# Kernel optimization log

Hardware: AMD Instinct MI355X
Metric: run time of the kernel (lower is better)

The kernel has to match this reference:

```python
import jax, jax.numpy as jnp
import numpy as np

N = 50000          # nodes
E_RAND = 800000    # random edges (plus N self-loops)
IN, HID, OUT = 128, 32, 32
HEADS = (4, 4, 6)
NEG_SLOPE = 0.2    # DGL GATConv default leaky_relu slope


def setup_inputs() -> dict:
    key = jax.random.key(0)
    ks = jax.random.split(key, 16)
    s = 0.05
    x = jax.random.normal(ks[0], (N, IN), jnp.float32)
    # random graph + self loops (SELF_LOOP=True in the source)
    src = jnp.concatenate([jax.random.randint(ks[1], (E_RAND,), 0, N),
                           jnp.arange(N)]).astype(jnp.int32)
    dst = jnp.concatenate([jax.random.randint(ks[2], (E_RAND,), 0, N),
                           jnp.arange(N)]).astype(jnp.int32)
    H0, H1, H2 = HEADS
    return dict(
        x=x, src=src, dst=dst,
        W1=jax.random.normal(ks[3], (IN, H0 * HID), jnp.float32) * s,
        al1=jax.random.normal(ks[4], (H0, HID), jnp.float32) * s,
        ar1=jax.random.normal(ks[5], (H0, HID), jnp.float32) * s,
        b1=jnp.zeros((H0 * HID,), jnp.float32),
        W2=jax.random.normal(ks[6], (H0 * HID, H1 * HID), jnp.float32) * s,
        al2=jax.random.normal(ks[7], (H1, HID), jnp.float32) * s,
        ar2=jax.random.normal(ks[8], (H1, HID), jnp.float32) * s,
        b2=jnp.zeros((H1 * HID,), jnp.float32),
        W3=jax.random.normal(ks[9], (H1 * HID, H2 * OUT), jnp.float32) * s,
        al3=jax.random.normal(ks[10], (H2, OUT), jnp.float32) * s,
        ar3=jax.random.normal(ks[11], (H2, OUT), jnp.float32) * s,
        b3=jnp.zeros((H2 * OUT,), jnp.float32),
        resW3=jax.random.normal(ks[12], (H1 * HID, H2 * OUT), jnp.float32) * s,
    )


def gat_layer(h, src, dst, W, al, ar, b, residual=None, act_relu=True):
    """One DGL-style GATConv: fc -> per-edge leaky_relu attention -> edge
    softmax over incoming edges -> weighted scatter-sum -> (+res) + bias -> act."""
    n = h.shape[0]
    H, out = al.shape
    feat = (h @ W).reshape(n, H, out)                 # [N,H,out]
    el = jnp.sum(feat * al, axis=-1)                  # [N,H]
    er = jnp.sum(feat * ar, axis=-1)                  # [N,H]
    e = jax.nn.leaky_relu(el[src] + er[dst], NEG_SLOPE)  # [E,H]
    emax = jax.ops.segment_max(e, dst, num_segments=n)   # [N,H]
    ex = jnp.exp(e - emax[dst])                       # [E,H]
    denom = jax.ops.segment_sum(ex, dst, num_segments=n) # [N,H]
    alpha = ex / jnp.maximum(denom[dst], 1e-9)        # [E,H]
    msg = feat[src] * alpha[..., None]                # [E,H,out]
    rst = jax.ops.segment_sum(msg, dst, num_segments=n)  # [N,H,out]
    if residual is not None:
        rst = rst + residual
    rst = rst + b.reshape(1, H, out)
    return jax.nn.relu(rst) if act_relu else rst


def reference(x, src, dst, W1, al1, ar1, b1, W2, al2, ar2, b2,
              W3, al3, ar3, b3, resW3):
    n = x.shape[0]
    # layer 1: no residual, relu, flatten heads
    h1 = gat_layer(x, src, dst, W1, al1, ar1, b1).reshape(n, -1)
    # layer 2: residual is Identity (in_dim == heads*hid), relu, flatten
    res2 = h1.reshape(n, HEADS[1], HID)
    h2 = gat_layer(h1, src, dst, W2, al2, ar2, b2, residual=res2).reshape(n, -1)
    # layer 3: residual via linear projection (dims differ), no activation, mean heads
    res3 = (h2 @ resW3).reshape(n, HEADS[2], OUT)
    h3 = gat_layer(h2, src, dst, W3, al3, ar3, b3, residual=res3, act_relu=False)
    return h3.mean(axis=1)
```

## Files before the change

kernel.cpp:

```cpp
#include <hip/hip_runtime.h>
#include <math.h>


typedef _Float16 v8h __attribute__((ext_vector_type(8)));
typedef float f32x4 __attribute__((ext_vector_type(4)));

__device__ __host__ inline int pack_off(int n, int k) {
    return ((n >> 4) << 11) | ((k >> 5) << 9) | (((k >> 3) & 3) << 7) | ((n & 15) << 3) | (k & 7);
}


__global__ void hist_kernel(const int* __restrict__ dst, int E, int* __restrict__ deg) {
    int i = blockIdx.x * blockDim.x + threadIdx.x;
    if (i < E) atomicAdd(&deg[dst[i]], 1);
}

__global__ void scan_phaseA(const int* __restrict__ deg, int n, int* __restrict__ bsum) {
    __shared__ int red[4];
    int t = threadIdx.x;
    int base = blockIdx.x * 2048 + t * 8;
    int s = 0;
    #pragma unroll
    for (int q = 0; q < 8; q++) { int i = base + q; if (i < n) s += deg[i]; }
    #pragma unroll
    for (int off = 1; off < 64; off <<= 1) s += __shfl_xor(s, off);
    if ((t & 63) == 0) red[t >> 6] = s;
    __syncthreads();
    if (t == 0) bsum[blockIdx.x] = red[0] + red[1] + red[2] + red[3];
}

__global__ void scan_phaseB(int* __restrict__ bsum, int nb) {
    int lane = threadIdx.x & 63;
    int v = (lane < nb) ? bsum[lane] : 0;
    int inc = v;
    #pragma unroll
    for (int off = 1; off < 64; off <<= 1) {
        int u = __shfl_up(inc, off);
        if (lane >= off) inc += u;
    }
    int ex = inc - v;
    if (lane < nb) bsum[lane] = ex;
}

__global__ void scan_phaseC(const int* __restrict__ deg, int n, const int* __restrict__ bsum,
                            int* __restrict__ row_start, int E) {
    __shared__ int wsum[4];
    int t = threadIdx.x;
    int lane = t & 63, wv = t >> 6;
    int base = blockIdx.x * 2048 + t * 8;
    int v[8]; int s = 0;
    #pragma unroll
    for (int q = 0; q < 8; q++) { int i = base + q; v[q] = (i < n) ? deg[i] : 0; s += v[q]; }
    int inc = s;
    #pragma unroll
    for (int off = 1; off < 64; off <<= 1) {
        int u = __shfl_up(inc, off);
        if (lane >= off) inc += u;
    }
    if (lane == 63) wsum[wv] = inc;
    __syncthreads();
    int woff = 0;
    for (int w = 0; w < wv; w++) woff += wsum[w];
    int run = inc - s + woff + bsum[blockIdx.x];
    #pragma unroll
    for (int q = 0; q < 8; q++) {
        int i = base + q;
        if (i < n) row_start[i] = run;
        run += v[q];
    }
    if (blockIdx.x == 0 && t == 0) row_start[n] = E;
}

__global__ void fill_kernel(const int* __restrict__ src, const int* __restrict__ dst, int E,
                            const int* __restrict__ row_start, int* __restrict__ cursor,
                            int* __restrict__ csr_src) {
    int i = blockIdx.x * blockDim.x + threadIdx.x;
    if (i < E) {
        int d = dst[i];
        int pos = atomicAdd(&cursor[d], 1);
        csr_src[row_start[d] + pos] = src[i];
    }
}


__global__ void wsplit_all(const float* __restrict__ W1, const float* __restrict__ W2,
                           const float* __restrict__ W3, const float* __restrict__ Wr,
                           _Float16* __restrict__ o) {
    int i = blockIdx.x * blockDim.x + threadIdx.x;
    if (i >= 61440) return;
    float v; int ohi, stride, po;
    if (i < 16384) {
        int e = i, c = e >> 7, k = e & 127;
        v = W1[(size_t)k * 128 + c]; ohi = 0; stride = 16384; po = pack_off(c, k);
    } else if (i < 32768) {
        int e = i - 16384, c = e >> 7, k = e & 127;
        v = W2[(size_t)k * 128 + c]; ohi = 32768; stride = 16384; po = pack_off(c, k);
    } else if (i < 57344) {
        int e = i - 32768, c = e >> 7, k = e & 127;
        v = W3[(size_t)k * 192 + c]; ohi = 65536; stride = 28672; po = pack_off(c, k);
    } else {
        int e = i - 57344, c = e >> 7, k = e & 127;
        float s = 0.f;
        #pragma unroll
        for (int h = 0; h < 6; h++) s += Wr[(size_t)k * 192 + h * 32 + c];
        v = s * (1.0f / 6.0f);
        ohi = 65536; stride = 28672; po = 24576 + pack_off(c, k);
    }
    _Float16 hv = (_Float16)v;
    o[ohi + po] = hv;
    o[ohi + stride + po] = (_Float16)(v - (float)hv);
}


__global__ void splitx_kernel(const float* __restrict__ x, _Float16* __restrict__ hi,
                              _Float16* __restrict__ lo, int N, int PT) {
    int i = blockIdx.x * blockDim.x + threadIdx.x;
    if (i >= PT * 2048) return;
    int mt = i >> 11, r = i & 2047;
    int q4 = r >> 9, quad = (r >> 7) & 3, ln = (r >> 3) & 15, j = r & 7;
    int n = mt * 16 + ln, k = q4 * 32 + quad * 8 + j;
    float v = (n < N) ? x[(size_t)n * 128 + k] : 0.f;
    _Float16 h = (_Float16)v;
    hi[i] = h;
    lo[i] = (_Float16)(v - (float)h);
}


template <int CC, int H>
__global__ __launch_bounds__(256, 4) void mfma_fc(
    const _Float16* __restrict__ Ahi, const _Float16* __restrict__ Alo,
    const _Float16* __restrict__ Bhi, const _Float16* __restrict__ Blo,
    const float* __restrict__ al, const float* __restrict__ ar,
    _Float16* __restrict__ feat_out,
    float* __restrict__ el, float* __restrict__ er, int N) {
    constexpr int TILES = CC / 16;
    int t = threadIdx.x;
    int wave = t >> 6, lane = t & 63;
    int ln = lane & 15, quad = lane >> 4;
    int mt = blockIdx.x * 4 + wave;

    f32x4 acc[TILES];
    #pragma unroll
    for (int i = 0; i < TILES; i++) acc[i] = (f32x4){0.f, 0.f, 0.f, 0.f};

    const _Float16* pa_h = Ahi + (size_t)mt * 2048 + lane * 8;
    const _Float16* pa_l = Alo + (size_t)mt * 2048 + lane * 8;

    #pragma unroll
    for (int q4 = 0; q4 < 4; q4++) {
        v8h ah = *(const v8h*)(pa_h + q4 * 512);
        v8h av = *(const v8h*)(pa_l + q4 * 512);
        #pragma unroll
        for (int tt = 0; tt < TILES; tt++) {
            size_t boff = (size_t)tt * 2048 + q4 * 512 + lane * 8;
            v8h bh = *(const v8h*)(Bhi + boff);
            v8h bl = *(const v8h*)(Blo + boff);
            acc[tt] = __builtin_amdgcn_mfma_f32_16x16x32_f16(av, bh, acc[tt], 0, 0, 0);
            acc[tt] = __builtin_amdgcn_mfma_f32_16x16x32_f16(ah, bl, acc[tt], 0, 0, 0);
            acc[tt] = __builtin_amdgcn_mfma_f32_16x16x32_f16(ah, bh, acc[tt], 0, 0, 0);
        }
    }

    #pragma unroll
    for (int tt = 0; tt < TILES; tt++) {
        int n = tt * 16 + ln;
        int head = n >> 5, wi = n & 31;
        _Float16* fo = feat_out + (size_t)head * N * 32;
        #pragma unroll
        for (int r = 0; r < 4; r++) {
            int m = mt * 16 + quad * 4 + r;
            if (m < N) fo[(size_t)m * 32 + wi] = (_Float16)acc[tt][r];
        }
    }
    #pragma unroll
    for (int hg = 0; hg < H; hg++) {
        float a0 = al[hg * 32 + ln], a1 = al[hg * 32 + 16 + ln];
        float r0 = ar[hg * 32 + ln], r1 = ar[hg * 32 + 16 + ln];
        #pragma unroll
        for (int r = 0; r < 4; r++) {
            float pl = acc[2 * hg][r] * a0 + acc[2 * hg + 1][r] * a1;
            float pr = acc[2 * hg][r] * r0 + acc[2 * hg + 1][r] * r1;
            #pragma unroll
            for (int off = 1; off < 16; off <<= 1) {
                pl += __shfl_xor(pl, off);
                pr += __shfl_xor(pr, off);
            }
            int m = mt * 16 + quad * 4 + r;
            if (ln == 0 && m < N) {
                el[(size_t)hg * N + m] = pl;
                er[(size_t)hg * N + m] = pr;
            }
        }
    }
}


__global__ __launch_bounds__(256, 3) void mfma_fc3(
    const _Float16* __restrict__ Ahi, const _Float16* __restrict__ Alo,
    const _Float16* __restrict__ Bhi, const _Float16* __restrict__ Blo,
    const float* __restrict__ al, const float* __restrict__ ar,
    const float* __restrict__ b3,
    _Float16* __restrict__ feat_out, float* __restrict__ out,
    float* __restrict__ el, float* __restrict__ er, int N) {
    constexpr int H = 6, TILES = 14;
    int t = threadIdx.x;
    int wave = t >> 6, lane = t & 63;
    int ln = lane & 15, quad = lane >> 4;
    int mt = blockIdx.x * 4 + wave;

    f32x4 acc[TILES];
    #pragma unroll
    for (int i = 0; i < TILES; i++) acc[i] = (f32x4){0.f, 0.f, 0.f, 0.f};

    const _Float16* pa_h = Ahi + (size_t)mt * 2048 + lane * 8;
    const _Float16* pa_l = Alo + (size_t)mt * 2048 + lane * 8;

    #pragma unroll
    for (int q4 = 0; q4 < 4; q4++) {
        v8h ah = *(const v8h*)(pa_h + q4 * 512);
        v8h av = *(const v8h*)(pa_l + q4 * 512);
        #pragma unroll
        for (int tt = 0; tt < TILES; tt++) {
            size_t boff = (size_t)tt * 2048 + q4 * 512 + lane * 8;
            v8h bh = *(const v8h*)(Bhi + boff);
            v8h bl = *(const v8h*)(Blo + boff);
            acc[tt] = __builtin_amdgcn_mfma_f32_16x16x32_f16(av, bh, acc[tt], 0, 0, 0);
            acc[tt] = __builtin_amdgcn_mfma_f32_16x16x32_f16(ah, bl, acc[tt], 0, 0, 0);
            acc[tt] = __builtin_amdgcn_mfma_f32_16x16x32_f16(ah, bh, acc[tt], 0, 0, 0);
        }
    }

    #pragma unroll
    for (int tt = 0; tt < 12; tt++) {
        int n = tt * 16 + ln;
        #pragma unroll
        for (int r = 0; r < 4; r++) {
            int m = mt * 16 + quad * 4 + r;
            if (m < N) feat_out[(size_t)m * 192 + n] = (_Float16)acc[tt][r];
        }
    }
    #pragma unroll
    for (int tt = 12; tt < 14; tt++) {
        int n32 = (tt - 12) * 16 + ln;
        float bm = (b3[n32] + b3[32 + n32] + b3[64 + n32] + b3[96 + n32] +
                    b3[128 + n32] + b3[160 + n32]) * (1.0f / 6.0f);
        #pragma unroll
        for (int r = 0; r < 4; r++) {
            int m = mt * 16 + quad * 4 + r;
            if (m < N) out[(size_t)m * 32 + n32] = acc[tt][r] + bm;
        }
    }
    #pragma unroll
    for (int hg = 0; hg < H; hg++) {
        float a0 = al[hg * 32 + ln], a1 = al[hg * 32 + 16 + ln];
        float r0 = ar[hg * 32 + ln], r1 = ar[hg * 32 + 16 + ln];
        #pragma unroll
        for (int r = 0; r < 4; r++) {
            float pl = acc[2 * hg][r] * a0 + acc[2 * hg + 1][r] * a1;
            float pr = acc[2 * hg][r] * r0 + acc[2 * hg + 1][r] * r1;
            #pragma unroll
            for (int off = 1; off < 16; off <<= 1) {
                pl += __shfl_xor(pl, off);
                pr += __shfl_xor(pr, off);
            }
            int m = mt * 16 + quad * 4 + r;
            if (ln == 0 && m < N) {
                el[(size_t)hg * N + m] = pl;
                er[(size_t)hg * N + m] = pr;
            }
        }
    }
}


template <int RES>
__global__ __launch_bounds__(256) void gat_agg_q(
        const _Float16* __restrict__ feat_planes, const float* __restrict__ el,
        const float* __restrict__ er, const int* __restrict__ row_start,
        const int* __restrict__ csr_src, const float* __restrict__ bias,
        const _Float16* __restrict__ res_hi, const _Float16* __restrict__ res_lo,
        _Float16* __restrict__ out_hi, _Float16* __restrict__ out_lo,
        int N, int NB16) {
    constexpr int H = 4;
    unsigned b = blockIdx.x;
    unsigned C = (unsigned)(NB16 * H) >> 3;
    unsigned t = (b & 7u) * C + (b >> 3);
    int h  = (int)(t / (unsigned)NB16);
    int ng = (int)(t - (unsigned)h * (unsigned)NB16);
    int wv = threadIdx.x >> 6, lane = threadIdx.x & 63;
    int slice = lane >> 4, sl = lane & 15;
    int q = sl & 3;
    int g = sl >> 2;
    int n = ng * 16 + wv * 4 + slice;
    bool valid = (n < N);
    int nc = valid ? n : (N - 1);

    int start = row_start[nc];
    int end   = valid ? row_start[nc + 1] : start;
    float er_h = er[(size_t)h * N + nc];
    const float* el_h = el + (size_t)h * N;
    const _Float16* fbase = feat_planes + (size_t)h * N * 32 + q * 8;

    float acc[8];
    #pragma unroll
    for (int i = 0; i < 8; i++) acc[i] = 0.f;
    float wsum = 0.f;

    int j = start + g;
    for (; j + 4 < end; j += 8) {
        int s0 = csr_src[j];
        int s1 = csr_src[j + 4];
        float e0 = el_h[s0] + er_h;
        float e1 = el_h[s1] + er_h;
        e0 = (e0 >= 0.f) ? e0 : 0.2f * e0;
        e1 = (e1 >= 0.f) ? e1 : 0.2f * e1;
        float w0 = __expf(e0);
        float w1 = __expf(e1);
        v8h v0 = *(const v8h*)(fbase + (size_t)s0 * 32);
        v8h v1 = *(const v8h*)(fbase + (size_t)s1 * 32);
        wsum += w0 + w1;
        #pragma unroll
        for (int i = 0; i < 8; i++) acc[i] += w0 * (float)v0[i] + w1 * (float)v1[i];
    }
    if (j < end) {
        int s0 = csr_src[j];
        float e0 = el_h[s0] + er_h;
        e0 = (e0 >= 0.f) ? e0 : 0.2f * e0;
        float w0 = __expf(e0);
        v8h v0 = *(const v8h*)(fbase + (size_t)s0 * 32);
        wsum += w0;
        #pragma unroll
        for (int i = 0; i < 8; i++) acc[i] += w0 * (float)v0[i];
    }

    #pragma unroll
    for (int off = 4; off < 16; off <<= 1) {
        #pragma unroll
        for (int i = 0; i < 8; i++) acc[i] += __shfl_xor(acc[i], off);
        wsum += __shfl_xor(wsum, off);
    }

    float inv = 1.0f / fmaxf(wsum, 1e-9f);
    float4 bv0 = *(const float4*)(bias + h * 32 + q * 8);
    float4 bv1 = *(const float4*)(bias + h * 32 + q * 8 + 4);
    float r[8];
    r[0] = acc[0] * inv + bv0.x; r[1] = acc[1] * inv + bv0.y;
    r[2] = acc[2] * inv + bv0.z; r[3] = acc[3] * inv + bv0.w;
    r[4] = acc[4] * inv + bv1.x; r[5] = acc[5] * inv + bv1.y;
    r[6] = acc[6] * inv + bv1.z; r[7] = acc[7] * inv + bv1.w;

    if constexpr (RES == 1) {
        int off = pack_off(nc, h * 32 + q * 8);
        v8h rh = *(const v8h*)(res_hi + off);
        v8h rl = *(const v8h*)(res_lo + off);
        #pragma unroll
        for (int i = 0; i < 8; i++) r[i] += (float)rh[i] + (float)rl[i];
    }
    #pragma unroll
    for (int i = 0; i < 8; i++) r[i] = fmaxf(r[i], 0.f);

    if (g == 0 && valid) {
        int po = pack_off(n, h * 32 + q * 8);
        v8h hh, ll;
        #pragma unroll
        for (int i = 0; i < 8; i++) {
            hh[i] = (_Float16)r[i];
            ll[i] = (_Float16)(r[i] - (float)hh[i]);
        }
        *(v8h*)(out_hi + po) = hh;
        *(v8h*)(out_lo + po) = ll;
    }
}


__global__ __launch_bounds__(256) void gat_agg_mean6p(
        const _Float16* __restrict__ feat, const float* __restrict__ el,
        const float* __restrict__ er, const int* __restrict__ row_start,
        const int* __restrict__ csr_src, float* __restrict__ out, int N) {
    constexpr int H = 6, ROW = 192, LPG = 24, G = 2;
    int wv = threadIdx.x >> 6, lane = threadIdx.x & 63;
    int n = blockIdx.x * 4 + wv;
    if (n >= N) return;

    int d8 = lane % LPG;
    int g  = lane / LPG;
    int hd = d8 >> 2, qb = d8 & 3;

    int start = row_start[n], end = row_start[n + 1];
    float er_hd = er[(size_t)hd * N + n];
    const float* el_h = el + (size_t)hd * N;
    const _Float16* fbase = feat + 8 * d8;

    float acc[8];
    #pragma unroll
    for (int q = 0; q < 8; q++) acc[q] = 0.f;
    float wsum = 0.f;

    int j = (g < G) ? (start + g) : end;
    for (; j + 3 * G < end; j += 4 * G) {
        int s0 = csr_src[j];
        int s1 = csr_src[j + G];
        int s2 = csr_src[j + 2 * G];
        int s3 = csr_src[j + 3 * G];
        float e0 = el_h[s0] + er_hd;
        float e1 = el_h[s1] + er_hd;
        float e2 = el_h[s2] + er_hd;
        float e3 = el_h[s3] + er_hd;
        e0 = (e0 >= 0.f) ? e0 : 0.2f * e0;
        e1 = (e1 >= 0.f) ? e1 : 0.2f * e1;
        e2 = (e2 >= 0.f) ? e2 : 0.2f * e2;
        e3 = (e3 >= 0.f) ? e3 : 0.2f * e3;
        float w0 = __expf(e0);
        float w1 = __expf(e1);
        float w2 = __expf(e2);
        float w3 = __expf(e3);
        v8h v0 = *(const v8h*)(fbase + (size_t)s0 * ROW);
        v8h v1 = *(const v8h*)(fbase + (size_t)s1 * ROW);
        v8h v2 = *(const v8h*)(fbase + (size_t)s2 * ROW);
        v8h v3 = *(const v8h*)(fbase + (size_t)s3 * ROW);
        wsum += (w0 + w1) + (w2 + w3);
        #pragma unroll
        for (int q = 0; q < 8; q++)
            acc[q] += (w0 * (float)v0[q] + w1 * (float)v1[q]) +
                      (w2 * (float)v2[q] + w3 * (float)v3[q]);
    }
    for (; j < end; j += G) {
        int s0 = csr_src[j];
        float e0 = el_h[s0] + er_hd;
        e0 = (e0 >= 0.f) ? e0 : 0.2f * e0;
        float w0 = __expf(e0);
        v8h v0 = *(const v8h*)(fbase + (size_t)s0 * ROW);
        wsum += w0;
        #pragma unroll
        for (int q = 0; q < 8; q++) acc[q] += w0 * (float)v0[q];
    }

    #pragma unroll
    for (int q = 0; q < 8; q++) acc[q] += __shfl(acc[q], lane + 24);
    wsum += __shfl(wsum, lane + 24);

    float inv = 1.0f / fmaxf(wsum, 1e-9f);
    float r[8];
    #pragma unroll
    for (int q = 0; q < 8; q++) r[q] = acc[q] * inv;

    float s[8];
    #pragma unroll
    for (int q = 0; q < 8; q++) {
        s[q] = r[q];
        #pragma unroll
        for (int hh2 = 1; hh2 < H; hh2++) s[q] += __shfl(r[q], qb + 4 * hh2);
    }
    if (lane < 4) {
        const float sc = 1.0f / 6.0f;
        float4 rm0 = *(const float4*)(out + (size_t)n * 32 + 8 * lane);
        float4 rm1 = *(const float4*)(out + (size_t)n * 32 + 8 * lane + 4);
        *(float4*)(out + (size_t)n * 32 + 8 * lane) =
            make_float4(s[0] * sc + rm0.x, s[1] * sc + rm0.y,
                        s[2] * sc + rm0.z, s[3] * sc + rm0.w);
        *(float4*)(out + (size_t)n * 32 + 8 * lane + 4) =
            make_float4(s[4] * sc + rm1.x, s[5] * sc + rm1.y,
                        s[6] * sc + rm1.z, s[7] * sc + rm1.w);
    }
}


extern "C" void kernel_launch(void* const* d_in, const int* in_sizes, int n_in,
                              void* d_out, int out_size, void* d_ws, size_t ws_size,
                              hipStream_t stream) {
    const float* x    = (const float*)d_in[0];
    const int*   src  = (const int*)d_in[1];
    const int*   dst  = (const int*)d_in[2];
    const float* W1   = (const float*)d_in[3];
    const float* al1  = (const float*)d_in[4];
    const float* ar1  = (const float*)d_in[5];
    const float* b1   = (const float*)d_in[6];
    const float* W2   = (const float*)d_in[7];
    const float* al2  = (const float*)d_in[8];
    const float* ar2  = (const float*)d_in[9];
    const float* b2   = (const float*)d_in[10];
    const float* W3   = (const float*)d_in[11];
    const float* al3  = (const float*)d_in[12];
    const float* ar3  = (const float*)d_in[13];
    const float* b3   = (const float*)d_in[14];
    const float* resW3= (const float*)d_in[15];
    float* out = (float*)d_out;

    const int N = in_sizes[0] / 128;
    const int E = in_sizes[1];
    const int TILES16 = (N + 15) / 16;
    const int PT = (TILES16 + 3) & ~3;
    const int NB = PT / 4;
    const int NSB = (N + 2047) / 2048;
    const int NB16 = (TILES16 + 3) & ~3;

    float* fws  = (float*)d_ws;
    float* elb  = fws;
    float* erb  = elb + (size_t)N * 6;
    _Float16* feat_h = (_Float16*)(erb + (size_t)N * 6);
    _Float16* xh_hi  = feat_h + (size_t)N * 192;
    _Float16* xh_lo  = xh_hi + (size_t)PT * 2048;
    _Float16* h1_hi  = xh_lo + (size_t)PT * 2048;
    _Float16* h1_lo  = h1_hi + (size_t)PT * 2048;
    _Float16* wts    = h1_lo + (size_t)PT * 2048;
    int* deg       = (int*)(wts + 122880);
    int* row_start = deg + N;
    int* bsum      = row_start + (N + 1);
    int* csr_src   = bsum + 64;

    const _Float16* W1h = wts;
    const _Float16* W1l = wts + 16384;
    const _Float16* W2h = wts + 32768;
    const _Float16* W2l = wts + 49152;
    const _Float16* B3h = wts + 65536;
    const _Float16* B3l = wts + 94208;

    hipMemsetAsync(deg, 0, (size_t)N * sizeof(int), stream);
    hist_kernel<<<dim3((E + 255) / 256), dim3(256), 0, stream>>>(dst, E, deg);
    scan_phaseA<<<dim3(NSB), dim3(256), 0, stream>>>(deg, N, bsum);
    scan_phaseB<<<dim3(1), dim3(64), 0, stream>>>(bsum, NSB);
    scan_phaseC<<<dim3(NSB), dim3(256), 0, stream>>>(deg, N, bsum, row_start, E);
    hipMemsetAsync(deg, 0, (size_t)N * sizeof(int), stream);
    fill_kernel<<<dim3((E + 255) / 256), dim3(256), 0, stream>>>(src, dst, E, row_start, deg, csr_src);
    wsplit_all<<<dim3(240), dim3(256), 0, stream>>>(W1, W2, W3, resW3, wts);
    splitx_kernel<<<dim3((PT * 2048 + 255) / 256), dim3(256), 0, stream>>>(x, xh_hi, xh_lo, N, PT);

    mfma_fc<128, 4><<<dim3(NB), dim3(256), 0, stream>>>(
        xh_hi, xh_lo, W1h, W1l, al1, ar1, feat_h, elb, erb, N);
    gat_agg_q<0><<<dim3(NB16 * 4), dim3(256), 0, stream>>>(
        feat_h, elb, erb, row_start, csr_src, b1,
        nullptr, nullptr, h1_hi, h1_lo, N, NB16);

    mfma_fc<128, 4><<<dim3(NB), dim3(256), 0, stream>>>(
        h1_hi, h1_lo, W2h, W2l, al2, ar2, feat_h, elb, erb, N);
    gat_agg_q<1><<<dim3(NB16 * 4), dim3(256), 0, stream>>>(
        feat_h, elb, erb, row_start, csr_src, b2,
        h1_hi, h1_lo, xh_hi, xh_lo, N, NB16);

    mfma_fc3<<<dim3(NB), dim3(256), 0, stream>>>(
        xh_hi, xh_lo, B3h, B3l, al3, ar3, b3, feat_h, out, elb, erb, N);
    gat_agg_mean6p<<<dim3((N + 3) / 4), dim3(256), 0, stream>>>(
        feat_h, elb, erb, row_start, csr_src, out, N);
}
```

Measured before the change: 425.5 us.

## Precompute per-edge layer-3 attention weights in a separate edge-parallel kernel

The CSR fill now also records the destination node of each edge. The layer-3 projection kernel stores el/er node-major with 8 floats per node, so one source or destination row is a vectorized load. A new edge-parallel kernel computes leaky_relu and exp for all 6 heads per edge into a buffer that reuses the dead h1 storage. The layer-3 aggregation then reads those precomputed weights instead of gathering el per edge and evaluating exp inline. This removes scattered el gathers and exp work from the aggregation, at the cost of an extra launch and roughly 20MB of per-edge weight traffic written and read back, plus a larger workspace.

Result: slower. 434.3 us (+2.1%).

```diff
diff --git a/kernel.cpp b/kernel.cpp
--- a/kernel.cpp
+++ b/kernel.cpp
@@ -73,12 +73,14 @@
 
 __global__ void fill_kernel(const int* __restrict__ src, const int* __restrict__ dst, int E,
                             const int* __restrict__ row_start, int* __restrict__ cursor,
-                            int* __restrict__ csr_src) {
+                            int* __restrict__ csr_src, int* __restrict__ csr_dst) {
     int i = blockIdx.x * blockDim.x + threadIdx.x;
     if (i < E) {
         int d = dst[i];
         int pos = atomicAdd(&cursor[d], 1);
-        csr_src[row_start[d] + pos] = src[i];
+        int at = row_start[d] + pos;
+        csr_src[at] = src[i];
+        csr_dst[at] = d;
     }
 }
 
@@ -201,7 +203,7 @@
     const float* __restrict__ al, const float* __restrict__ ar,
     const float* __restrict__ b3,
     _Float16* __restrict__ feat_out, float* __restrict__ out,
-    float* __restrict__ el, float* __restrict__ er, int N) {
+    float* __restrict__ el8, float* __restrict__ er8, int N) {
     constexpr int H = 6, TILES = 14;
     int t = threadIdx.x;
     int wave = t >> 6, lane = t & 63;
@@ -265,10 +267,32 @@
             }
             int m = mt * 16 + quad * 4 + r;
             if (ln == 0 && m < N) {
-                el[(size_t)hg * N + m] = pl;
-                er[(size_t)hg * N + m] = pr;
+                el8[(size_t)m * 8 + hg] = pl;
+                er8[(size_t)m * 8 + hg] = pr;
             }
         }
+    }
+}
+
+
+__global__ void wexp_l3(const int* __restrict__ csr_src, const int* __restrict__ csr_dst,
+                        const float* __restrict__ el8, const float* __restrict__ er8,
+                        float* __restrict__ wexp, int E) {
+    int i = blockIdx.x * blockDim.x + threadIdx.x;
+    if (i >= E) return;
+    int s = csr_src[i], d = csr_dst[i];
+    float4 a0 = *(const float4*)(el8 + (size_t)s * 8);
+    float2 a1 = *(const float2*)(el8 + (size_t)s * 8 + 4);
+    float4 b0 = *(const float4*)(er8 + (size_t)d * 8);
+    float2 b1 = *(const float2*)(er8 + (size_t)d * 8 + 4);
+    float e[6] = {a0.x + b0.x, a0.y + b0.y, a0.z + b0.z, a0.w + b0.w,
+                  a1.x + b1.x, a1.y + b1.y};
+    float* wp = wexp + (size_t)i * 6;
+    #pragma unroll
+    for (int h = 0; h < 6; h++) {
+        float v = e[h];
+        v = (v >= 0.f) ? v : 0.2f * v;
+        wp[h] = __expf(v);
     }
 }
 
@@ -373,10 +397,10 @@
 }
 
 
-__global__ __launch_bounds__(256) void gat_agg_mean6p(
-        const _Float16* __restrict__ feat, const float* __restrict__ el,
-        const float* __restrict__ er, const int* __restrict__ row_start,
-        const int* __restrict__ csr_src, float* __restrict__ out, int N) {
+__global__ __launch_bounds__(256) void gat_agg_mean6w(
+        const _Float16* __restrict__ feat, const float* __restrict__ wexp,
+        const int* __restrict__ row_start, const int* __restrict__ csr_src,
+        float* __restrict__ out, int N) {
     constexpr int H = 6, ROW = 192, LPG = 24, G = 2;
     int wv = threadIdx.x >> 6, lane = threadIdx.x & 63;
     int n = blockIdx.x * 4 + wv;
@@ -387,8 +411,6 @@
     int hd = d8 >> 2, qb = d8 & 3;
 
     int start = row_start[n], end = row_start[n + 1];
-    float er_hd = er[(size_t)hd * N + n];
-    const float* el_h = el + (size_t)hd * N;
     const _Float16* fbase = feat + 8 * d8;
 
     float acc[8];
@@ -402,18 +424,10 @@
         int s1 = csr_src[j + G];
         int s2 = csr_src[j + 2 * G];
         int s3 = csr_src[j + 3 * G];
-        float e0 = el_h[s0] + er_hd;
-        float e1 = el_h[s1] + er_hd;
-        float e2 = el_h[s2] + er_hd;
-        float e3 = el_h[s3] + er_hd;
-        e0 = (e0 >= 0.f) ? e0 : 0.2f * e0;
-        e1 = (e1 >= 0.f) ? e1 : 0.2f * e1;
-        e2 = (e2 >= 0.f) ? e2 : 0.2f * e2;
-        e3 = (e3 >= 0.f) ? e3 : 0.2f * e3;
-        float w0 = __expf(e0);
-        float w1 = __expf(e1);
-        float w2 = __expf(e2);
-        float w3 = __expf(e3);
+        float w0 = wexp[(size_t)j * 6 + hd];
+        float w1 = wexp[(size_t)(j + G) * 6 + hd];
+        float w2 = wexp[(size_t)(j + 2 * G) * 6 + hd];
+        float w3 = wexp[(size_t)(j + 3 * G) * 6 + hd];
         v8h v0 = *(const v8h*)(fbase + (size_t)s0 * ROW);
         v8h v1 = *(const v8h*)(fbase + (size_t)s1 * ROW);
         v8h v2 = *(const v8h*)(fbase + (size_t)s2 * ROW);
@@ -426,9 +440,7 @@
     }
     for (; j < end; j += G) {
         int s0 = csr_src[j];
-        float e0 = el_h[s0] + er_hd;
-        e0 = (e0 >= 0.f) ? e0 : 0.2f * e0;
-        float w0 = __expf(e0);
+        float w0 = wexp[(size_t)j * 6 + hd];
         v8h v0 = *(const v8h*)(fbase + (size_t)s0 * ROW);
         wsum += w0;
         #pragma unroll
@@ -507,6 +519,10 @@
     int* row_start = deg + N;
     int* bsum      = row_start + (N + 1);
     int* csr_src   = bsum + 64;
+    int* csr_dst   = csr_src + E;
+    float* el8     = (float*)(csr_dst + E);
+    float* er8     = el8 + (size_t)N * 8;
+    float* wexp    = (float*)h1_hi;
 
     const _Float16* W1h = wts;
     const _Float16* W1l = wts + 16384;
@@ -521,7 +537,8 @@
     scan_phaseB<<<dim3(1), dim3(64), 0, stream>>>(bsum, NSB);
     scan_phaseC<<<dim3(NSB), dim3(256), 0, stream>>>(deg, N, bsum, row_start, E);
     hipMemsetAsync(deg, 0, (size_t)N * sizeof(int), stream);
-    fill_kernel<<<dim3((E + 255) / 256), dim3(256), 0, stream>>>(src, dst, E, row_start, deg, csr_src);
+    fill_kernel<<<dim3((E + 255) / 256), dim3(256), 0, stream>>>(src, dst, E, row_start, deg,
+                                                                 csr_src, csr_dst);
     wsplit_all<<<dim3(240), dim3(256), 0, stream>>>(W1, W2, W3, resW3, wts);
     splitx_kernel<<<dim3((PT * 2048 + 255) / 256), dim3(256), 0, stream>>>(x, xh_hi, xh_lo, N, PT);
 
@@ -538,7 +555,9 @@
         h1_hi, h1_lo, xh_hi, xh_lo, N, NB16);
 
     mfma_fc3<<<dim3(NB), dim3(256), 0, stream>>>(
-        xh_hi, xh_lo, B3h, B3l, al3, ar3, b3, feat_h, out, elb, erb, N);
-    gat_agg_mean6p<<<dim3((N + 3) / 4), dim3(256), 0, stream>>>(
-        feat_h, elb, erb, row_start, csr_src, out, N);
-}
+        xh_hi, xh_lo, B3h, B3l, al3, ar3, b3, feat_h, out, el8, er8, N);
+    wexp_l3<<<dim3((E + 255) / 256), dim3(256), 0, stream>>>(
+        csr_src, csr_dst, el8, er8, wexp, E);
+    gat_agg_mean6w<<<dim3((N + 3) / 4), dim3(256), 0, stream>>>(
+        feat_h, wexp, row_start, csr_src, out, N);
+}
```
